# Kernel optimization log

Hardware: AMD Instinct MI355X
Metric: run time of the kernel (lower is better)

## Reference

```python
import jax, jax.numpy as jnp
import numpy as np

N = 100000
E = 1000000
F = 64

def setup_inputs() -> dict:
    key = jax.random.key(0)
    k1, k2, k3 = jax.random.split(key, 3)
    x = jax.random.normal(k1, (N, F), dtype=jnp.float32)
    edge_weight = jax.random.uniform(k2, (E,), dtype=jnp.float32)
    edge_index = jax.random.randint(k3, (2, E), 0, N, dtype=jnp.int64)
    return {"x": x, "edge_weight": edge_weight, "edge_index": edge_index, "num_nodes": N}

def reference(x, edge_weight, edge_index, num_nodes):
    # flow='source_to_target': j=0 (source, gathered), i=1 (target, scattered)
    src, dst = edge_index[0], edge_index[1]
    # message: gather source features, scale by edge weight -> [E, F]
    msg = edge_weight[:, None] * x[src]
    # aggregate: scatter_add into zero-initialized [num_nodes, F]
    out = jax.ops.segment_sum(msg, dst, num_segments=num_nodes)
    return out
```

## Files before the change

kernel.cpp:

```cpp
#include <hip/hip_runtime.h>


#define FDIM 64
#define BSHIFT 7
#define BNODES 128
#define BMAX 1024
#define SLOT 1536
#define SC_EPB 2048
#define SC_THREADS 512
#define SC_KPT (SC_EPB / SC_THREADS)
#define H_EPT 8
#define H_EPB (256 * H_EPT)
#define CAP 2048
#define A_THREADS 512
#define A_KPT (CAP / A_THREADS)

__global__ void __launch_bounds__(256)
scatter_edges_kernel(const float* __restrict__ x,
                     const float* __restrict__ w,
                     const int* __restrict__ src,
                     const int* __restrict__ dst,
                     float* __restrict__ out,
                     int E) {
    int gid = blockIdx.x * blockDim.x + threadIdx.x;
    int e = gid >> 4;
    int q = gid & 15;
    if (e >= E) return;
    int s = src[e];
    int d = dst[e];
    float we = w[e];
    const float4* xrow = reinterpret_cast<const float4*>(x + (size_t)s * FDIM);
    float4 v = xrow[q];
    float* o = out + (size_t)d * FDIM + q * 4;
    atomicAdd(o + 0, we * v.x);
    atomicAdd(o + 1, we * v.y);
    atomicAdd(o + 2, we * v.z);
    atomicAdd(o + 3, we * v.w);
}

__device__ __forceinline__ unsigned int bf16rn(float f) {
    unsigned int u = __float_as_uint(f);
    u += 0x7fffu + ((u >> 16) & 1u);
    return u >> 16;
}

__global__ void __launch_bounds__(256)
conv_bf16(const float* __restrict__ x, uint4* __restrict__ xb, int total8) {
    int i = blockIdx.x * 256 + threadIdx.x;
    if (i >= total8) return;
    const float4* p = reinterpret_cast<const float4*>(x) + (size_t)i * 2;
    float4 a = p[0], b = p[1];
    uint4 o;
    o.x = bf16rn(a.x) | (bf16rn(a.y) << 16);
    o.y = bf16rn(a.z) | (bf16rn(a.w) << 16);
    o.z = bf16rn(b.x) | (bf16rn(b.y) << 16);
    o.w = bf16rn(b.z) | (bf16rn(b.w) << 16);
    xb[i] = o;
}

__global__ void __launch_bounds__(256)
bucket_hist(const int* __restrict__ dst, int* __restrict__ bcnt, int E, int B) {
    __shared__ int h[BMAX];
    int t = threadIdx.x;
    for (int i = t; i < B; i += 256) h[i] = 0;
    __syncthreads();
    int base = blockIdx.x * H_EPB + t * H_EPT;
    if (base + H_EPT <= E) {
        int4 a = *reinterpret_cast<const int4*>(dst + base);
        int4 b = *reinterpret_cast<const int4*>(dst + base + 4);
        atomicAdd(&h[a.x >> BSHIFT], 1); atomicAdd(&h[a.y >> BSHIFT], 1);
        atomicAdd(&h[a.z >> BSHIFT], 1); atomicAdd(&h[a.w >> BSHIFT], 1);
        atomicAdd(&h[b.x >> BSHIFT], 1); atomicAdd(&h[b.y >> BSHIFT], 1);
        atomicAdd(&h[b.z >> BSHIFT], 1); atomicAdd(&h[b.w >> BSHIFT], 1);
    } else {
        for (int k = 0; k < H_EPT; ++k) {
            int e = base + k;
            if (e < E) atomicAdd(&h[dst[e] >> BSHIFT], 1);
        }
    }
    __syncthreads();
    for (int i = t; i < B; i += 256) if (h[i]) atomicAdd(&bcnt[i], h[i]);
}

__global__ void __launch_bounds__(1024)
bucket_scan(const int* __restrict__ bcnt, int* __restrict__ boff,
            int* __restrict__ cursor, int B, int E) {
    __shared__ int sh[1024];
    int t = threadIdx.x;
    int v = (t < B) ? bcnt[t] : 0;
    sh[t] = v;
    __syncthreads();
    for (int d = 1; d < 1024; d <<= 1) {
        int u = (t >= d) ? sh[t - d] : 0;
        __syncthreads();
        sh[t] += u;
        __syncthreads();
    }
    if (t < B) { int ex = sh[t] - v; boff[t] = ex; cursor[t] = ex; }
    if (t == 0) boff[B] = E;
}

__device__ __forceinline__ void scatter_body(
        const int* __restrict__ src, const int* __restrict__ dst,
        const float* __restrict__ w, int* __restrict__ cursor,
        int2* __restrict__ rec, int E, int B, int slot, int sblk) {
    __shared__ int2 lrec[SC_EPB];
    __shared__ unsigned short lbin[SC_EPB];
    __shared__ int h[BMAX];
    __shared__ int noff[BMAX];
    __shared__ int cbase[BMAX];
    __shared__ int wsum[SC_THREADS / 64];
    __shared__ int wexc[SC_THREADS / 64];
    int t = threadIdx.x;
    int lane = t & 63;
    int wid = t >> 6;
    for (int i = t; i < B; i += SC_THREADS) h[i] = 0;
    __syncthreads();

    int blk = sblk * SC_EPB;
    int cnt = E - blk; if (cnt > SC_EPB) cnt = SC_EPB;

    int bkt[SC_KPT]; int rnk[SC_KPT]; int pv[SC_KPT]; float wv[SC_KPT];
    int base = blk + t * SC_KPT;
    if (base + SC_KPT <= E) {
        int4 s4 = *reinterpret_cast<const int4*>(src + base);
        int4 d4 = *reinterpret_cast<const int4*>(dst + base);
        float4 w4 = *reinterpret_cast<const float4*>(w + base);
        int sv[SC_KPT] = { s4.x, s4.y, s4.z, s4.w };
        int dv[SC_KPT] = { d4.x, d4.y, d4.z, d4.w };
        wv[0] = w4.x; wv[1] = w4.y; wv[2] = w4.z; wv[3] = w4.w;
        #pragma unroll
        for (int k = 0; k < SC_KPT; ++k) {
            int bb = dv[k] >> BSHIFT;
            bkt[k] = bb;
            pv[k] = sv[k] | ((dv[k] & (BNODES - 1)) << 17);
            rnk[k] = atomicAdd(&h[bb], 1);
        }
    } else {
        #pragma unroll
        for (int k = 0; k < SC_KPT; ++k) {
            int e = base + k;
            if (e < E) {
                int d = dst[e];
                int bb = d >> BSHIFT;
                bkt[k] = bb;
                pv[k] = src[e] | ((d & (BNODES - 1)) << 17);
                wv[k] = w[e];
                rnk[k] = atomicAdd(&h[bb], 1);
            } else bkt[k] = -1;
        }
    }
    __syncthreads();

    int bpt = (B + SC_THREADS - 1) / SC_THREADS;
    int hv[2] = {0, 0};
    int s = 0;
    int i0 = t * bpt;
    for (int k = 0; k < bpt; ++k) {
        int i = i0 + k;
        if (i < B) { hv[k] = h[i]; s += hv[k]; }
    }
    int v = s;
    #pragma unroll
    for (int d = 1; d < 64; d <<= 1) {
        int u = __shfl_up(v, d);
        if (lane >= d) v += u;
    }
    if (lane == 63) wsum[wid] = v;
    __syncthreads();
    if (wid == 0 && lane < SC_THREADS / 64) {
        int wv2 = wsum[lane];
        int vv = wv2;
        #pragma unroll
        for (int d = 1; d < SC_THREADS / 64; d <<= 1) {
            int u = __shfl_up(vv, d, SC_THREADS / 64);
            if (lane >= d) vv += u;
        }
        wexc[lane] = vv - wv2;
    }
    __syncthreads();
    int run = wexc[wid] + (v - s);
    for (int k = 0; k < bpt; ++k) {
        int i = i0 + k;
        if (i < B) { noff[i] = run; run += hv[k]; }
    }
    __syncthreads();

    #pragma unroll
    for (int k = 0; k < SC_KPT; ++k) {
        if (bkt[k] >= 0) {
            int p = noff[bkt[k]] + rnk[k];
            int2 r; r.x = pv[k]; r.y = __float_as_int(wv[k]);
            lrec[p] = r;
            lbin[p] = (unsigned short)bkt[k];
        }
    }
    for (int i = t; i < B; i += SC_THREADS)
        if (h[i]) cbase[i] = atomicAdd(&cursor[i], h[i]);
    __syncthreads();

    if (slot > 0) {
        for (int i = t; i < cnt; i += SC_THREADS) {
            int b = lbin[i];
            int ofs = cbase[b] + (i - noff[b]);
            if (ofs >= slot) continue;
            rec[b * slot + ofs] = lrec[i];
        }
    } else {
        for (int i = t; i < cnt; i += SC_THREADS) {
            int b = lbin[i];
            rec[cbase[b] + (i - noff[b])] = lrec[i];
        }
    }
}

__global__ void __launch_bounds__(SC_THREADS)
fused_conv_scatter(const int* __restrict__ src, const int* __restrict__ dst,
                   const float* __restrict__ w, int* __restrict__ cursor,
                   int2* __restrict__ rec, int E, int B, int gridS,
                   const float* __restrict__ x, uint4* __restrict__ xb,
                   int total8) {
    if ((int)blockIdx.x >= gridS) {
        int i = ((int)blockIdx.x - gridS) * SC_THREADS + (int)threadIdx.x;
        if (i < total8) {
            const float4* p = reinterpret_cast<const float4*>(x) + (size_t)i * 2;
            float4 a = p[0], b = p[1];
            uint4 o;
            o.x = bf16rn(a.x) | (bf16rn(a.y) << 16);
            o.y = bf16rn(a.z) | (bf16rn(a.w) << 16);
            o.z = bf16rn(b.x) | (bf16rn(b.y) << 16);
            o.w = bf16rn(b.z) | (bf16rn(b.w) << 16);
            xb[i] = o;
        }
        return;
    }
    scatter_body(src, dst, w, cursor, rec, E, B, SLOT, (int)blockIdx.x);
}

__global__ void __launch_bounds__(SC_THREADS)
bucket_scatter(const int* __restrict__ src, const int* __restrict__ dst,
               const float* __restrict__ w, int* __restrict__ cursor,
               int2* __restrict__ rec, int E, int B) {
    scatter_body(src, dst, w, cursor, rec, E, B, 0, (int)blockIdx.x);
}

__device__ __forceinline__ void acc8(const uint4& u, float wv,
                                     float4& a0, float4& a1) {
    a0.x += wv * __uint_as_float(u.x << 16);
    a0.y += wv * __uint_as_float(u.x & 0xFFFF0000u);
    a0.z += wv * __uint_as_float(u.y << 16);
    a0.w += wv * __uint_as_float(u.y & 0xFFFF0000u);
    a1.x += wv * __uint_as_float(u.z << 16);
    a1.y += wv * __uint_as_float(u.z & 0xFFFF0000u);
    a1.z += wv * __uint_as_float(u.w << 16);
    a1.w += wv * __uint_as_float(u.w & 0xFFFF0000u);
}

__global__ void __launch_bounds__(A_THREADS)
bucket_sort_accum(const uint4* __restrict__ xb, const int2* __restrict__ rec,
                  const int* __restrict__ boff, const int* __restrict__ cursor,
                  int slot, float* __restrict__ out, int N) {
    __shared__ int2 lrec[CAP];
    __shared__ int nhist[BNODES];
    __shared__ int noff[BNODES];
    __shared__ int swtot;
    int b = blockIdx.x;
    int t = threadIdx.x;
    int g = t >> 3;
    int q = t & 7;
    int beg, end;
    if (slot > 0) {
        beg = b * slot;
        int c = cursor[b];
        if (c > slot) c = slot;
        if (c < 0) c = 0;
        end = beg + c;
    } else {
        beg = boff[b]; end = boff[b + 1];
    }

    float4 acc[2][2];
    #pragma unroll
    for (int j = 0; j < 2; ++j) {
        acc[j][0] = make_float4(0.f, 0.f, 0.f, 0.f);
        acc[j][1] = make_float4(0.f, 0.f, 0.f, 0.f);
    }

    for (int pos = beg; pos < end; pos += CAP) {
        int cnt = end - pos; if (cnt > CAP) cnt = CAP;
        if (t < BNODES) nhist[t] = 0;
        __syncthreads();
        int2 myrec[A_KPT]; int myrank[A_KPT]; int mybin[A_KPT];
        #pragma unroll
        for (int k = 0; k < A_KPT; ++k) {
            int i = k * A_THREADS + t;
            if (i < cnt) {
                int2 r = rec[pos + i];
                int bin = (r.x >> 17) & (BNODES - 1);
                myrec[k] = r;
                mybin[k] = bin;
                myrank[k] = atomicAdd(&nhist[bin], 1);
            } else mybin[k] = -1;
        }
        __syncthreads();
        int hv = 0, v = 0;
        if (t < BNODES) {
            hv = nhist[t];
            v = hv;
            #pragma unroll
            for (int d = 1; d < 64; d <<= 1) {
                int u = __shfl_up(v, d);
                if ((t & 63) >= d) v += u;
            }
        }
        if (t == 63) swtot = v;
        __syncthreads();
        if (t >= 64 && t < BNODES) v += swtot;
        if (t < BNODES) noff[t] = v - hv;
        __syncthreads();
        #pragma unroll
        for (int k = 0; k < A_KPT; ++k)
            if (mybin[k] >= 0) lrec[noff[mybin[k]] + myrank[k]] = myrec[k];
        __syncthreads();

        #pragma unroll
        for (int j = 0; j < 2; ++j) {
            int n = j * 64 + g;
            int sb = noff[n];
            int se = sb + nhist[n];
            int i = sb;
            for (; i + 4 <= se; i += 4) {
                int2 r0 = lrec[i + 0], r1 = lrec[i + 1];
                int2 r2 = lrec[i + 2], r3 = lrec[i + 3];
                uint4 u0 = xb[(size_t)(r0.x & 0x1FFFF) * 8 + q];
                uint4 u1 = xb[(size_t)(r1.x & 0x1FFFF) * 8 + q];
                uint4 u2 = xb[(size_t)(r2.x & 0x1FFFF) * 8 + q];
                uint4 u3 = xb[(size_t)(r3.x & 0x1FFFF) * 8 + q];
                acc8(u0, __int_as_float(r0.y), acc[j][0], acc[j][1]);
                acc8(u1, __int_as_float(r1.y), acc[j][0], acc[j][1]);
                acc8(u2, __int_as_float(r2.y), acc[j][0], acc[j][1]);
                acc8(u3, __int_as_float(r3.y), acc[j][0], acc[j][1]);
            }
            for (; i < se; ++i) {
                int2 r = lrec[i];
                uint4 u = xb[(size_t)(r.x & 0x1FFFF) * 8 + q];
                acc8(u, __int_as_float(r.y), acc[j][0], acc[j][1]);
            }
        }
        __syncthreads();
    }

    int nodeBase = b << BSHIFT;
    #pragma unroll
    for (int j = 0; j < 2; ++j) {
        int row = nodeBase + j * 64 + g;
        if (row < N) {
            float4* o = reinterpret_cast<float4*>(out + ((size_t)row << 6)) + q * 2;
            o[0] = acc[j][0];
            o[1] = acc[j][1];
        }
    }
}

extern "C" void kernel_launch(void* const* d_in, const int* in_sizes, int n_in,
                              void* d_out, int out_size, void* d_ws, size_t ws_size,
                              hipStream_t stream) {
    const float* x  = (const float*)d_in[0];
    const float* w  = (const float*)d_in[1];
    const int* eidx = (const int*)d_in[2];
    int E = in_sizes[1];
    int N = out_size / FDIM;
    const int* src = eidx;
    const int* dst = eidx + E;
    float* out = (float*)d_out;

    int B = (N + BNODES - 1) >> BSHIFT;
    int total8 = N * (FDIM / 8);
    int gridS = (E + SC_EPB - 1) / SC_EPB;
    size_t xb_bytes = (size_t)N * FDIM * sizeof(unsigned short);

    if (B <= BMAX && N <= (1 << 17)) {
        {
            int* cursor = (int*)d_ws;
            size_t rec_off = ((size_t)B * sizeof(int) + 15) & ~(size_t)15;
            int2* rec = (int2*)((char*)d_ws + rec_off);
            size_t xb_off = (rec_off + (size_t)B * SLOT * sizeof(int2) + 15) & ~(size_t)15;
            uint4* xb = (uint4*)((char*)d_ws + xb_off);
            size_t need = xb_off + xb_bytes;
            if (ws_size >= need) {
                hipMemsetAsync(cursor, 0, (size_t)B * sizeof(int), stream);
                int gridC = (total8 + SC_THREADS - 1) / SC_THREADS;
                fused_conv_scatter<<<gridS + gridC, SC_THREADS, 0, stream>>>(
                    src, dst, w, cursor, rec, E, B, gridS, x, xb, total8);
                bucket_sort_accum<<<B, A_THREADS, 0, stream>>>(
                    xb, rec, (const int*)nullptr, cursor, SLOT, out, N);
                return;
            }
        }
        {
            int* bcnt   = (int*)d_ws;
            int* boff   = bcnt + B;
            int* cursor = boff + B + 1;
            size_t rec_off = (((size_t)(3 * B + 1)) * sizeof(int) + 15) & ~(size_t)15;
            int2* rec = (int2*)((char*)d_ws + rec_off);
            size_t xb_off = (rec_off + (size_t)E * sizeof(int2) + 15) & ~(size_t)15;
            uint4* xb = (uint4*)((char*)d_ws + xb_off);
            size_t need = xb_off + xb_bytes;
            if (ws_size >= need) {
                hipMemsetAsync(bcnt, 0, (size_t)B * sizeof(int), stream);
                conv_bf16<<<(total8 + 255) / 256, 256, 0, stream>>>(x, xb, total8);
                int gridH = (E + H_EPB - 1) / H_EPB;
                bucket_hist<<<gridH, 256, 0, stream>>>(dst, bcnt, E, B);
                bucket_scan<<<1, 1024, 0, stream>>>(bcnt, boff, cursor, B, E);
                bucket_scatter<<<gridS, SC_THREADS, 0, stream>>>(src, dst, w, cursor, rec, E, B);
                bucket_sort_accum<<<B, A_THREADS, 0, stream>>>(xb, rec, boff,
                                                               cursor, 0, out, N);
                return;
            }
        }
    }

    hipMemsetAsync(out, 0, (size_t)out_size * sizeof(float), stream);
    int grid = (E * 16 + 255) / 256;
    scatter_edges_kernel<<<grid, 256, 0, stream>>>(x, w, src, dst, out, E);
}
```

Measured before the change: 144.0 us.

## Fold cursor init into bf16 conversion, split fused scatter, double edges per block

Replaces the hipMemsetAsync on the bucket cursors by zeroing them inside the bf16 conversion kernel. The conversion is no longer fused into the scatter launch and now runs as its own kernel. Each scatter block now handles 4096 edges, 8 per thread, loaded as two int4/float4 chunks. This removes a memset launch and halves the number of scatter blocks, but adds a separate kernel launch and serialises conversion before scatter. Larger blocks raise register and LDS pressure and reduce parallelism.

```diff
diff --git a/kernel.cpp b/kernel.cpp
--- a/kernel.cpp
+++ b/kernel.cpp
@@ -6,7 +6,7 @@
 #define BNODES 128
 #define BMAX 1024
 #define SLOT 1536
-#define SC_EPB 2048
+#define SC_EPB 4096
 #define SC_THREADS 512
 #define SC_KPT (SC_EPB / SC_THREADS)
 #define H_EPT 8
@@ -45,8 +45,10 @@
 }
 
 __global__ void __launch_bounds__(256)
-conv_bf16(const float* __restrict__ x, uint4* __restrict__ xb, int total8) {
+conv_bf16(const float* __restrict__ x, uint4* __restrict__ xb, int total8,
+          int* __restrict__ cursor, int B, int doInit) {
     int i = blockIdx.x * 256 + threadIdx.x;
+    if (doInit && i < B) cursor[i] = 0;
     if (i >= total8) return;
     const float4* p = reinterpret_cast<const float4*>(x) + (size_t)i * 2;
     float4 a = p[0], b = p[1];
@@ -123,18 +125,23 @@
     int bkt[SC_KPT]; int rnk[SC_KPT]; int pv[SC_KPT]; float wv[SC_KPT];
     int base = blk + t * SC_KPT;
     if (base + SC_KPT <= E) {
-        int4 s4 = *reinterpret_cast<const int4*>(src + base);
-        int4 d4 = *reinterpret_cast<const int4*>(dst + base);
-        float4 w4 = *reinterpret_cast<const float4*>(w + base);
-        int sv[SC_KPT] = { s4.x, s4.y, s4.z, s4.w };
-        int dv[SC_KPT] = { d4.x, d4.y, d4.z, d4.w };
-        wv[0] = w4.x; wv[1] = w4.y; wv[2] = w4.z; wv[3] = w4.w;
-        #pragma unroll
-        for (int k = 0; k < SC_KPT; ++k) {
-            int bb = dv[k] >> BSHIFT;
-            bkt[k] = bb;
-            pv[k] = sv[k] | ((dv[k] & (BNODES - 1)) << 17);
-            rnk[k] = atomicAdd(&h[bb], 1);
+        #pragma unroll
+        for (int c = 0; c < SC_KPT / 4; ++c) {
+            int4 s4 = *reinterpret_cast<const int4*>(src + base + c * 4);
+            int4 d4 = *reinterpret_cast<const int4*>(dst + base + c * 4);
+            float4 w4 = *reinterpret_cast<const float4*>(w + base + c * 4);
+            int sv[4] = { s4.x, s4.y, s4.z, s4.w };
+            int dv[4] = { d4.x, d4.y, d4.z, d4.w };
+            float wl[4] = { w4.x, w4.y, w4.z, w4.w };
+            #pragma unroll
+            for (int j = 0; j < 4; ++j) {
+                int k = c * 4 + j;
+                int bb = dv[j] >> BSHIFT;
+                bkt[k] = bb;
+                pv[k] = sv[j] | ((dv[j] & (BNODES - 1)) << 17);
+                wv[k] = wl[j];
+                rnk[k] = atomicAdd(&h[bb], 1);
+            }
         }
     } else {
         #pragma unroll
@@ -215,32 +222,16 @@
 }
 
 __global__ void __launch_bounds__(SC_THREADS)
-fused_conv_scatter(const int* __restrict__ src, const int* __restrict__ dst,
-                   const float* __restrict__ w, int* __restrict__ cursor,
-                   int2* __restrict__ rec, int E, int B, int gridS,
-                   const float* __restrict__ x, uint4* __restrict__ xb,
-                   int total8) {
-    if ((int)blockIdx.x >= gridS) {
-        int i = ((int)blockIdx.x - gridS) * SC_THREADS + (int)threadIdx.x;
-        if (i < total8) {
-            const float4* p = reinterpret_cast<const float4*>(x) + (size_t)i * 2;
-            float4 a = p[0], b = p[1];
-            uint4 o;
-            o.x = bf16rn(a.x) | (bf16rn(a.y) << 16);
-            o.y = bf16rn(a.z) | (bf16rn(a.w) << 16);
-            o.z = bf16rn(b.x) | (bf16rn(b.y) << 16);
-            o.w = bf16rn(b.z) | (bf16rn(b.w) << 16);
-            xb[i] = o;
-        }
-        return;
-    }
+bucket_scatter_slot(const int* __restrict__ src, const int* __restrict__ dst,
+                    const float* __restrict__ w, int* __restrict__ cursor,
+                    int2* __restrict__ rec, int E, int B) {
     scatter_body(src, dst, w, cursor, rec, E, B, SLOT, (int)blockIdx.x);
 }
 
 __global__ void __launch_bounds__(SC_THREADS)
-bucket_scatter(const int* __restrict__ src, const int* __restrict__ dst,
-               const float* __restrict__ w, int* __restrict__ cursor,
-               int2* __restrict__ rec, int E, int B) {
+bucket_scatter_exact(const int* __restrict__ src, const int* __restrict__ dst,
+                     const float* __restrict__ w, int* __restrict__ cursor,
+                     int2* __restrict__ rec, int E, int B) {
     scatter_body(src, dst, w, cursor, rec, E, B, 0, (int)blockIdx.x);
 }
 
@@ -376,6 +367,7 @@
 
     int B = (N + BNODES - 1) >> BSHIFT;
     int total8 = N * (FDIM / 8);
+    int gridC = (total8 + 255) / 256;
     int gridS = (E + SC_EPB - 1) / SC_EPB;
     size_t xb_bytes = (size_t)N * FDIM * sizeof(unsigned short);
 
@@ -388,10 +380,9 @@
             uint4* xb = (uint4*)((char*)d_ws + xb_off);
             size_t need = xb_off + xb_bytes;
             if (ws_size >= need) {
-                hipMemsetAsync(cursor, 0, (size_t)B * sizeof(int), stream);
-                int gridC = (total8 + SC_THREADS - 1) / SC_THREADS;
-                fused_conv_scatter<<<gridS + gridC, SC_THREADS, 0, stream>>>(
-                    src, dst, w, cursor, rec, E, B, gridS, x, xb, total8);
+                conv_bf16<<<gridC, 256, 0, stream>>>(x, xb, total8, cursor, B, 1);
+                bucket_scatter_slot<<<gridS, SC_THREADS, 0, stream>>>(
+                    src, dst, w, cursor, rec, E, B);
                 bucket_sort_accum<<<B, A_THREADS, 0, stream>>>(
                     xb, rec, (const int*)nullptr, cursor, SLOT, out, N);
                 return;
@@ -408,11 +399,12 @@
             size_t need = xb_off + xb_bytes;
             if (ws_size >= need) {
                 hipMemsetAsync(bcnt, 0, (size_t)B * sizeof(int), stream);
-                conv_bf16<<<(total8 + 255) / 256, 256, 0, stream>>>(x, xb, total8);
+                conv_bf16<<<gridC, 256, 0, stream>>>(x, xb, total8, cursor, B, 0);
                 int gridH = (E + H_EPB - 1) / H_EPB;
                 bucket_hist<<<gridH, 256, 0, stream>>>(dst, bcnt, E, B);
                 bucket_scan<<<1, 1024, 0, stream>>>(bcnt, boff, cursor, B, E);
-                bucket_scatter<<<gridS, SC_THREADS, 0, stream>>>(src, dst, w, cursor, rec, E, B);
+                bucket_scatter_exact<<<gridS, SC_THREADS, 0, stream>>>(
+                    src, dst, w, cursor, rec, E, B);
                 bucket_sort_accum<<<B, A_THREADS, 0, stream>>>(xb, rec, boff,
                                                                cursor, 0, out, N);
                 return;
```

After: 133.0 us. -7.7%, faster.
